# Performance work log

Measured on AMD Instinct MI355X. Metric: run time of the kernel, lower is better.

Reference implementation:

```python
import jax, jax.numpy as jnp
import numpy as np

EPS = 1e-8  # torch.cosine_similarity eps
TEMPERATURE = 1.0


def setup_inputs() -> dict:
    key = jax.random.key(0)
    ks = jax.random.split(key, 12)
    B = 16384
    inp = {
        "user_ids": jax.random.randint(ks[0], (B, 8), 0, 100000),
        "item_ids": jax.random.randint(ks[1], (B, 4), 0, 50000),
        "sample_weight": jax.random.uniform(ks[2], (B,), jnp.float32, 0.01, 1.0),
        "user_table": jax.random.normal(ks[3], (100000, 64), jnp.float32) * 0.05,
        "item_table": jax.random.normal(ks[4], (50000, 64), jnp.float32) * 0.05,
        "uW1": jax.random.normal(ks[5], (512, 256), jnp.float32) * 0.04,
        "ub1": jnp.zeros((256,), jnp.float32),
        "uW2": jax.random.normal(ks[6], (256, 128), jnp.float32) * 0.06,
        "ub2": jnp.zeros((128,), jnp.float32),
        "iW1": jax.random.normal(ks[7], (256, 256), jnp.float32) * 0.06,
        "ib1": jnp.zeros((256,), jnp.float32),
        "iW2": jax.random.normal(ks[8], (256, 128), jnp.float32) * 0.06,
        "ib2": jnp.zeros((128,), jnp.float32),
        "n_neg": 3,
    }
    return inp


def _tower(ids, table, W1, b1, W2, b2):
    # embedding lookup [B, F, D] -> concat -> [B, F*D], then 2-layer relu MLP
    B = ids.shape[0]
    e = table[ids].reshape(B, -1)
    h = jax.nn.relu(e @ W1 + b1)
    return jax.nn.relu(h @ W2 + b2)


def reference(user_ids, item_ids, sample_weight, user_table, item_table,
              uW1, ub1, uW2, ub2, iW1, ib1, iW2, ib2, n_neg):
    u = _tower(user_ids, user_table, uW1, ub1, uW2, ub2)  # [B, 128]
    v = _tower(item_ids, item_table, iW1, ib1, iW2, ib2)  # [B, 128]
    # cosine similarity per row (torch eps clamp on norms)
    un = jnp.maximum(jnp.linalg.norm(u, axis=1), EPS)
    vn = jnp.maximum(jnp.linalg.norm(v, axis=1), EPS)
    y = jnp.sum(u * v, axis=1) / (un * vn)
    # sampling-bias correction
    y = y - jnp.log(sample_weight)
    # vectorized wrap-around in-batch negative gather:
    # scores[i] = [y[i], y[(i+1)%B], ..., y[(i+n_neg)%B]]
    B = y.shape[0]
    idx = (jnp.arange(B)[:, None] + jnp.arange(n_neg + 1)[None, :]) % B
    scores = y[idx] / TEMPERATURE  # [B, 1+n_neg]
    return scores
```

## Files before the change

### kernel.cpp

```cpp
#include <hip/hip_runtime.h>
#include <math.h>

#define CEPS 1e-8f

typedef __attribute__((ext_vector_type(8))) short bf16x8;
typedef __attribute__((ext_vector_type(4))) float f32x4;
typedef __attribute__((ext_vector_type(4))) unsigned int u32x4;

__device__ __forceinline__ unsigned short f2bf(float f) {
    unsigned u = __builtin_bit_cast(unsigned, f);
    u += 0x7fffu + ((u >> 16) & 1u);
    return (unsigned short)(u >> 16);
}

__global__ __launch_bounds__(256)
void pack_all(const float* __restrict__ uW1, const float* __restrict__ uW2,
              const float* __restrict__ iW1, const float* __restrict__ iW2,
              unsigned short* __restrict__ o1, unsigned short* __restrict__ o2,
              unsigned short* __restrict__ o3, unsigned short* __restrict__ o4)
{
    int g = blockIdx.x * 256 + threadIdx.x;
    const float* src; unsigned short* dst; int N; int base;
    if (g < 16384)      { src = uW1; dst = o1; N = 256; base = 0;     }
    else if (g < 20480) { src = uW2; dst = o2; N = 128; base = 16384; }
    else if (g < 28672) { src = iW1; dst = o3; N = 256; base = 20480; }
    else                { src = iW2; dst = o4; N = 128; base = 28672; }
    int i = g - base;
    int kg = i / N, n = i - kg * N;
    unsigned short tmp[8];
    #pragma unroll
    for (int j = 0; j < 8; ++j)
        tmp[j] = f2bf(src[(kg * 8 + j) * N + n]);
    *reinterpret_cast<bf16x8*>(dst + ((size_t)i << 3)) =
        *reinterpret_cast<bf16x8*>(tmp);
}


template<int F>
__device__ __forceinline__ void stage_emb(const int* __restrict__ ids,
                                          const float* __restrict__ table,
                                          unsigned short* e_s, int row0, int tid)
{
    constexpr int FC = F * 8;
    constexpr int IT = (64 * FC) / 1024;
    int idv[IT];
    #pragma unroll
    for (int it = 0; it < IT; ++it) {
        int c = tid + it * 1024;
        int r = c / FC, f = (c % FC) >> 3;
        idv[it] = ids[(row0 + r) * F + f];
    }
    #pragma unroll
    for (int it = 0; it < IT; ++it) {
        int c = tid + it * 1024;
        int r = c / FC, rem = c % FC, ci = rem & 7;
        const float* src = table + (size_t)idv[it] * 64 + ci * 8;
        float4 aa = *reinterpret_cast<const float4*>(src);
        float4 bb = *reinterpret_cast<const float4*>(src + 4);
        u32x4 pk;
        pk.x = f2bf(aa.x) | ((unsigned)f2bf(aa.y) << 16);
        pk.y = f2bf(aa.z) | ((unsigned)f2bf(aa.w) << 16);
        pk.z = f2bf(bb.x) | ((unsigned)f2bf(bb.y) << 16);
        pk.w = f2bf(bb.z) | ((unsigned)f2bf(bb.w) << 16);
        int byte = r * (F * 128) + rem * 16;
        byte ^= (r & 7) << 4;
        *reinterpret_cast<u32x4*>(reinterpret_cast<char*>(e_s) + byte) = pk;
    }
}

template<int KB>
__device__ __forceinline__ bf16x8 loadA(const unsigned short* s, int rowbase,
                                        int ks, int m, int l15, int l4)
{
    int row = rowbase + m * 16 + l15;
    int byte = row * (KB * 2) + ks * 64 + l4 * 16;
    byte ^= (row & 7) << 4;
    return *reinterpret_cast<const bf16x8*>(
               reinterpret_cast<const char*>(s) + byte);
}

template<int K1>
__device__ __forceinline__ void gemm1(
    const unsigned short* e_s, unsigned short* h_s,
    const unsigned short* __restrict__ W1p, const float* __restrict__ b1,
    int l15, int l4, int w, bf16x8 b0)
{
    constexpr int NKS = K1 / 32;
    const int col = w * 16 + l15;
    f32x4 acc[4];
    #pragma unroll
    for (int m = 0; m < 4; ++m) acc[m] = (f32x4){0.f, 0.f, 0.f, 0.f};

    const unsigned short* Wbase = W1p + (((l4 * 256) + col) << 3);
    bf16x8 aB[2][4], bB[2];
    bB[0] = b0;
    #pragma unroll
    for (int m = 0; m < 4; ++m) aB[0][m] = loadA<K1>(e_s, 0, 0, m, l15, l4);

    #pragma unroll
    for (int ks = 0; ks < NKS; ++ks) {
        const int cur = ks & 1, nxt = cur ^ 1;
        if (ks + 1 < NKS) {
            #pragma unroll
            for (int m = 0; m < 4; ++m)
                aB[nxt][m] = loadA<K1>(e_s, 0, ks + 1, m, l15, l4);
            bB[nxt] = *reinterpret_cast<const bf16x8*>(Wbase + (ks + 1) * 8192);
        }
        #pragma unroll
        for (int m = 0; m < 4; ++m)
            acc[m] = __builtin_amdgcn_mfma_f32_16x16x32_bf16(
                         aB[cur][m], bB[cur], acc[m], 0, 0, 0);
    }
    const float bias = b1[col];
    #pragma unroll
    for (int m = 0; m < 4; ++m)
        #pragma unroll
        for (int r = 0; r < 4; ++r) {
            int row = m * 16 + l4 * 4 + r;
            float v = acc[m][r] + bias;
            v = v > 0.f ? v : 0.f;
            int byte = (row * 256 + col) * 2;
            byte ^= (row & 7) << 4;
            *reinterpret_cast<unsigned short*>(
                reinterpret_cast<char*>(h_s) + byte) = f2bf(v);
        }
}

__device__ __forceinline__ void gemm2(
    const unsigned short* h_s, const unsigned short* __restrict__ W2p,
    f32x4 (&acc)[2], int l15, int l4, int w, bf16x8 b0)
{
    const int col = (w & 7) * 16 + l15;
    const int rowbase = (w >> 3) * 32;
    #pragma unroll
    for (int m = 0; m < 2; ++m) acc[m] = (f32x4){0.f, 0.f, 0.f, 0.f};

    const unsigned short* Wbase = W2p + (((l4 * 128) + col) << 3);
    bf16x8 aB[2][2], bB[2];
    bB[0] = b0;
    #pragma unroll
    for (int m = 0; m < 2; ++m) aB[0][m] = loadA<256>(h_s, rowbase, 0, m, l15, l4);

    #pragma unroll
    for (int ks = 0; ks < 8; ++ks) {
        const int cur = ks & 1, nxt = cur ^ 1;
        if (ks + 1 < 8) {
            #pragma unroll
            for (int m = 0; m < 2; ++m)
                aB[nxt][m] = loadA<256>(h_s, rowbase, ks + 1, m, l15, l4);
            bB[nxt] = *reinterpret_cast<const bf16x8*>(Wbase + (ks + 1) * 4096);
        }
        #pragma unroll
        for (int m = 0; m < 2; ++m)
            acc[m] = __builtin_amdgcn_mfma_f32_16x16x32_bf16(
                         aB[cur][m], bB[cur], acc[m], 0, 0, 0);
    }
}

__global__ __launch_bounds__(1024, 4)
void fused_sbc(const int* __restrict__ user_ids,  const int* __restrict__ item_ids,
               const float* __restrict__ user_table, const float* __restrict__ item_table,
               const unsigned short* __restrict__ uW1p, const float* __restrict__ ub1,
               const unsigned short* __restrict__ uW2p, const float* __restrict__ ub2,
               const unsigned short* __restrict__ iW1p, const float* __restrict__ ib1,
               const unsigned short* __restrict__ iW2p, const float* __restrict__ ib2,
               const float* __restrict__ sw, float* __restrict__ out,
               int B, int nn1)
{
    __shared__ unsigned short e_u[64 * 512];
    __shared__ unsigned short e_i[64 * 256];
    __shared__ unsigned short h_s[64 * 256];
    __shared__ float red[8][64][3];

    const int tid  = threadIdx.x;
    const int lane = tid & 63;
    const int w    = tid >> 6;
    const int l15  = lane & 15, l4 = lane >> 4;
    const int row0 = blockIdx.x * 64;

    bf16x8 b0u1 = *reinterpret_cast<const bf16x8*>(
                      uW1p + ((l4 * 256 + w * 16 + l15) << 3));
    stage_emb<8>(user_ids, user_table, e_u, row0, tid);
    stage_emb<4>(item_ids, item_table, e_i, row0, tid);
    __syncthreads();

    gemm1<512>(e_u, h_s, uW1p, ub1, l15, l4, w, b0u1);
    bf16x8 b0u2 = *reinterpret_cast<const bf16x8*>(
                      uW2p + ((l4 * 128 + (w & 7) * 16 + l15) << 3));
    bf16x8 b0i1 = *reinterpret_cast<const bf16x8*>(
                      iW1p + ((l4 * 256 + w * 16 + l15) << 3));
    __syncthreads();

    f32x4 accU[2];
    gemm2(h_s, uW2p, accU, l15, l4, w, b0u2);
    __syncthreads();

    gemm1<256>(e_i, h_s, iW1p, ib1, l15, l4, w, b0i1);
    bf16x8 b0i2 = *reinterpret_cast<const bf16x8*>(
                      iW2p + ((l4 * 128 + (w & 7) * 16 + l15) << 3));
    __syncthreads();

    f32x4 accV[2];
    gemm2(h_s, iW2p, accV, l15, l4, w, b0i2);

    const int col = (w & 7) * 16 + l15;
    const float bu = ub2[col];
    const float bv = ib2[col];
    float pd[8], pu[8], pv[8];
    #pragma unroll
    for (int m = 0; m < 2; ++m)
        #pragma unroll
        for (int r = 0; r < 4; ++r) {
            float uval = accU[m][r] + bu;
            float vval = accV[m][r] + bv;
            uval = uval > 0.f ? uval : 0.f;
            vval = vval > 0.f ? vval : 0.f;
            int i = m * 4 + r;
            pd[i] = uval * vval;
            pu[i] = uval * uval;
            pv[i] = vval * vval;
        }
    #pragma unroll
    for (int off = 1; off < 16; off <<= 1) {
        #pragma unroll
        for (int i = 0; i < 8; ++i) {
            pd[i] += __shfl_xor(pd[i], off);
            pu[i] += __shfl_xor(pu[i], off);
            pv[i] += __shfl_xor(pv[i], off);
        }
    }
    if (l15 == 0) {
        const int rowbase = (w >> 3) * 32;
        #pragma unroll
        for (int m = 0; m < 2; ++m)
            #pragma unroll
            for (int r = 0; r < 4; ++r) {
                int row = rowbase + m * 16 + l4 * 4 + r;
                int i = m * 4 + r;
                red[w & 7][row][0] = pd[i];
                red[w & 7][row][1] = pu[i];
                red[w & 7][row][2] = pv[i];
            }
    }
    __syncthreads();

    if (tid < 64) {
        int row = tid;
        float d = 0.f, su = 0.f, sv = 0.f;
        #pragma unroll
        for (int cg = 0; cg < 8; ++cg) {
            d  += red[cg][row][0];
            su += red[cg][row][1];
            sv += red[cg][row][2];
        }
        float un = fmaxf(sqrtf(su), CEPS);
        float vn = fmaxf(sqrtf(sv), CEPS);
        int grow = row0 + row;
        float yv = d / (un * vn) - logf(sw[grow]);
        for (int j = 0; j < nn1; ++j) {
            int idx = grow - j;
            if (idx < 0) idx += B;
            out[idx * nn1 + j] = yv;
        }
    }
}

extern "C" void kernel_launch(void* const* d_in, const int* in_sizes, int n_in,
                              void* d_out, int out_size, void* d_ws, size_t ws_size,
                              hipStream_t stream)
{
    const int*   user_ids   = (const int*)  d_in[0];
    const int*   item_ids   = (const int*)  d_in[1];
    const float* sw         = (const float*)d_in[2];
    const float* user_table = (const float*)d_in[3];
    const float* item_table = (const float*)d_in[4];
    const float* uW1        = (const float*)d_in[5];
    const float* ub1        = (const float*)d_in[6];
    const float* uW2        = (const float*)d_in[7];
    const float* ub2        = (const float*)d_in[8];
    const float* iW1        = (const float*)d_in[9];
    const float* ib1        = (const float*)d_in[10];
    const float* iW2        = (const float*)d_in[11];
    const float* ib2        = (const float*)d_in[12];

    const int B   = in_sizes[2];
    const int nn1 = out_size / B;

    unsigned short* wp   = (unsigned short*)d_ws;
    unsigned short* uW1p = wp;
    unsigned short* uW2p = wp + 131072;
    unsigned short* iW1p = wp + 163840;
    unsigned short* iW2p = wp + 229376;
    float* out = (float*)d_out;

    pack_all<<<128, 256, 0, stream>>>(uW1, uW2, iW1, iW2,
                                      uW1p, uW2p, iW1p, iW2p);
    fused_sbc<<<B / 64, 1024, 0, stream>>>(user_ids, item_ids,
                                           user_table, item_table,
                                           uW1p, ub1, uW2p, ub2,
                                           iW1p, ib1, iW2p, ib2,
                                           sw, out, B, nn1);
}
```

Before: 33.57 us.

## Run user and item towers concurrently on separate wave halves

Splits the 16 waves into two roles: waves 0-7 run the user tower and waves 8-15 run the item tower at the same time, each on its own hidden buffer. Each wave now computes a wider tile (32 columns in layer 1, all 64 rows in layer 2), and the item tower output is passed to the user waves through LDS for the dot product. This removes two block-wide barriers and the serial user-then-item schedule, and gives each wave more MFMAs per A-fragment load. In exchange it uses more registers, drops the 4-blocks occupancy hint, and leaves the two towers with unequal work (K of 512 versus 256), so the item waves may sit idle.

Result: faster. 32.40 us (-3.5%).

```diff
diff --git a/kernel.cpp b/kernel.cpp
--- a/kernel.cpp
+++ b/kernel.cpp
@@ -69,10 +69,10 @@
 }
 
 template<int KB>
-__device__ __forceinline__ bf16x8 loadA(const unsigned short* s, int rowbase,
-                                        int ks, int m, int l15, int l4)
-{
-    int row = rowbase + m * 16 + l15;
+__device__ __forceinline__ bf16x8 loadA(const unsigned short* s, int ks, int m,
+                                        int l15, int l4)
+{
+    int row = m * 16 + l15;
     int byte = row * (KB * 2) + ks * 64 + l4 * 16;
     byte ^= (row & 7) << 4;
     return *reinterpret_cast<const bf16x8*>(
@@ -83,19 +83,22 @@
 __device__ __forceinline__ void gemm1(
     const unsigned short* e_s, unsigned short* h_s,
     const unsigned short* __restrict__ W1p, const float* __restrict__ b1,
-    int l15, int l4, int w, bf16x8 b0)
+    int l15, int l4, int wl, const bf16x8* b0)
 {
     constexpr int NKS = K1 / 32;
-    const int col = w * 16 + l15;
-    f32x4 acc[4];
-    #pragma unroll
-    for (int m = 0; m < 4; ++m) acc[m] = (f32x4){0.f, 0.f, 0.f, 0.f};
-
-    const unsigned short* Wbase = W1p + (((l4 * 256) + col) << 3);
-    bf16x8 aB[2][4], bB[2];
-    bB[0] = b0;
-    #pragma unroll
-    for (int m = 0; m < 4; ++m) aB[0][m] = loadA<K1>(e_s, 0, 0, m, l15, l4);
+    const int colbase = wl * 32;
+    f32x4 acc[4][2];
+    #pragma unroll
+    for (int m = 0; m < 4; ++m)
+        #pragma unroll
+        for (int n = 0; n < 2; ++n) acc[m][n] = (f32x4){0.f, 0.f, 0.f, 0.f};
+
+    const unsigned short* Wbase = W1p + (((l4 * 256) + colbase + l15) << 3);
+    bf16x8 aB[2][4], bB[2][2];
+    bB[0][0] = b0[0];
+    bB[0][1] = b0[1];
+    #pragma unroll
+    for (int m = 0; m < 4; ++m) aB[0][m] = loadA<K1>(e_s, 0, m, l15, l4);
 
     #pragma unroll
     for (int ks = 0; ks < NKS; ++ks) {
@@ -103,61 +106,69 @@
         if (ks + 1 < NKS) {
             #pragma unroll
             for (int m = 0; m < 4; ++m)
-                aB[nxt][m] = loadA<K1>(e_s, 0, ks + 1, m, l15, l4);
-            bB[nxt] = *reinterpret_cast<const bf16x8*>(Wbase + (ks + 1) * 8192);
+                aB[nxt][m] = loadA<K1>(e_s, ks + 1, m, l15, l4);
+            #pragma unroll
+            for (int n = 0; n < 2; ++n)
+                bB[nxt][n] = *reinterpret_cast<const bf16x8*>(
+                                 Wbase + (ks + 1) * 8192 + (n << 7));
+        }
+        #pragma unroll
+        for (int n = 0; n < 2; ++n)
+            #pragma unroll
+            for (int m = 0; m < 4; ++m)
+                acc[m][n] = __builtin_amdgcn_mfma_f32_16x16x32_bf16(
+                                aB[cur][m], bB[cur][n], acc[m][n], 0, 0, 0);
+    }
+    #pragma unroll
+    for (int n = 0; n < 2; ++n) {
+        int col = colbase + n * 16 + l15;
+        float bias = b1[col];
+        #pragma unroll
+        for (int m = 0; m < 4; ++m)
+            #pragma unroll
+            for (int r = 0; r < 4; ++r) {
+                int row = m * 16 + l4 * 4 + r;
+                float v = acc[m][n][r] + bias;
+                v = v > 0.f ? v : 0.f;
+                int byte = (row * 256 + col) * 2;
+                byte ^= (row & 7) << 4;
+                *reinterpret_cast<unsigned short*>(
+                    reinterpret_cast<char*>(h_s) + byte) = f2bf(v);
+            }
+    }
+}
+
+__device__ __forceinline__ void gemm2(
+    const unsigned short* h_s, const unsigned short* __restrict__ W2p,
+    f32x4 (&acc)[4], int l15, int l4, int wl, bf16x8 b0)
+{
+    const int col = wl * 16 + l15;
+    #pragma unroll
+    for (int m = 0; m < 4; ++m) acc[m] = (f32x4){0.f, 0.f, 0.f, 0.f};
+
+    const unsigned short* Wbase = W2p + (((l4 * 128) + col) << 3);
+    bf16x8 aB[2][4], bB[2];
+    bB[0] = b0;
+    #pragma unroll
+    for (int m = 0; m < 4; ++m) aB[0][m] = loadA<256>(h_s, 0, m, l15, l4);
+
+    #pragma unroll
+    for (int ks = 0; ks < 8; ++ks) {
+        const int cur = ks & 1, nxt = cur ^ 1;
+        if (ks + 1 < 8) {
+            #pragma unroll
+            for (int m = 0; m < 4; ++m)
+                aB[nxt][m] = loadA<256>(h_s, ks + 1, m, l15, l4);
+            bB[nxt] = *reinterpret_cast<const bf16x8*>(Wbase + (ks + 1) * 4096);
         }
         #pragma unroll
         for (int m = 0; m < 4; ++m)
             acc[m] = __builtin_amdgcn_mfma_f32_16x16x32_bf16(
                          aB[cur][m], bB[cur], acc[m], 0, 0, 0);
     }
-    const float bias = b1[col];
-    #pragma unroll
-    for (int m = 0; m < 4; ++m)
-        #pragma unroll
-        for (int r = 0; r < 4; ++r) {
-            int row = m * 16 + l4 * 4 + r;
-            float v = acc[m][r] + bias;
-            v = v > 0.f ? v : 0.f;
-            int byte = (row * 256 + col) * 2;
-            byte ^= (row & 7) << 4;
-            *reinterpret_cast<unsigned short*>(
-                reinterpret_cast<char*>(h_s) + byte) = f2bf(v);
-        }
-}
-
-__device__ __forceinline__ void gemm2(
-    const unsigned short* h_s, const unsigned short* __restrict__ W2p,
-    f32x4 (&acc)[2], int l15, int l4, int w, bf16x8 b0)
-{
-    const int col = (w & 7) * 16 + l15;
-    const int rowbase = (w >> 3) * 32;
-    #pragma unroll
-    for (int m = 0; m < 2; ++m) acc[m] = (f32x4){0.f, 0.f, 0.f, 0.f};
-
-    const unsigned short* Wbase = W2p + (((l4 * 128) + col) << 3);
-    bf16x8 aB[2][2], bB[2];
-    bB[0] = b0;
-    #pragma unroll
-    for (int m = 0; m < 2; ++m) aB[0][m] = loadA<256>(h_s, rowbase, 0, m, l15, l4);
-
-    #pragma unroll
-    for (int ks = 0; ks < 8; ++ks) {
-        const int cur = ks & 1, nxt = cur ^ 1;
-        if (ks + 1 < 8) {
-            #pragma unroll
-            for (int m = 0; m < 2; ++m)
-                aB[nxt][m] = loadA<256>(h_s, rowbase, ks + 1, m, l15, l4);
-            bB[nxt] = *reinterpret_cast<const bf16x8*>(Wbase + (ks + 1) * 4096);
-        }
-        #pragma unroll
-        for (int m = 0; m < 2; ++m)
-            acc[m] = __builtin_amdgcn_mfma_f32_16x16x32_bf16(
-                         aB[cur][m], bB[cur], acc[m], 0, 0, 0);
-    }
-}
-
-__global__ __launch_bounds__(1024, 4)
+}
+
+__global__ __launch_bounds__(1024)
 void fused_sbc(const int* __restrict__ user_ids,  const int* __restrict__ item_ids,
                const float* __restrict__ user_table, const float* __restrict__ item_table,
                const unsigned short* __restrict__ uW1p, const float* __restrict__ ub1,
@@ -167,80 +178,108 @@
                const float* __restrict__ sw, float* __restrict__ out,
                int B, int nn1)
 {
-    __shared__ unsigned short e_u[64 * 512];
-    __shared__ unsigned short e_i[64 * 256];
-    __shared__ unsigned short h_s[64 * 256];
-    __shared__ float red[8][64][3];
+    __shared__ __align__(16) unsigned short smem[81920];
+    unsigned short* e_u = smem;
+    unsigned short* e_i = smem + 32768;
+    unsigned short* h_u = smem + 49152;
+    unsigned short* h_i = smem + 65536;
+    float* V_lds = reinterpret_cast<float*>(smem);
+    float* red   = reinterpret_cast<float*>(smem + 32768);
 
     const int tid  = threadIdx.x;
     const int lane = tid & 63;
     const int w    = tid >> 6;
     const int l15  = lane & 15, l4 = lane >> 4;
+    const int role = w >> 3;
+    const int wl   = w & 7;
     const int row0 = blockIdx.x * 64;
 
-    bf16x8 b0u1 = *reinterpret_cast<const bf16x8*>(
-                      uW1p + ((l4 * 256 + w * 16 + l15) << 3));
+    const unsigned short* W1sel = role ? iW1p : uW1p;
+    const unsigned short* W2sel = role ? iW2p : uW2p;
+
+    bf16x8 b0g1[2];
+    {
+        const unsigned short* base = W1sel + ((l4 * 256 + wl * 32 + l15) << 3);
+        b0g1[0] = *reinterpret_cast<const bf16x8*>(base);
+        b0g1[1] = *reinterpret_cast<const bf16x8*>(base + 128);
+    }
     stage_emb<8>(user_ids, user_table, e_u, row0, tid);
     stage_emb<4>(item_ids, item_table, e_i, row0, tid);
     __syncthreads();
 
-    gemm1<512>(e_u, h_s, uW1p, ub1, l15, l4, w, b0u1);
-    bf16x8 b0u2 = *reinterpret_cast<const bf16x8*>(
-                      uW2p + ((l4 * 128 + (w & 7) * 16 + l15) << 3));
-    bf16x8 b0i1 = *reinterpret_cast<const bf16x8*>(
-                      iW1p + ((l4 * 256 + w * 16 + l15) << 3));
+    if (role == 0) gemm1<512>(e_u, h_u, uW1p, ub1, l15, l4, wl, b0g1);
+    else           gemm1<256>(e_i, h_i, iW1p, ib1, l15, l4, wl, b0g1);
+    bf16x8 b0g2 = *reinterpret_cast<const bf16x8*>(
+                      W2sel + ((l4 * 128 + wl * 16 + l15) << 3));
     __syncthreads();
 
-    f32x4 accU[2];
-    gemm2(h_s, uW2p, accU, l15, l4, w, b0u2);
+    f32x4 acc2[4];
+    if (role == 0) gemm2(h_u, uW2p, acc2, l15, l4, wl, b0g2);
+    else           gemm2(h_i, iW2p, acc2, l15, l4, wl, b0g2);
+
+    const int col = wl * 16 + l15;
+
+    if (role == 1) {
+        const float bv = ib2[col];
+        float pv[16];
+        #pragma unroll
+        for (int m = 0; m < 4; ++m)
+            #pragma unroll
+            for (int r = 0; r < 4; ++r) {
+                float vv = acc2[m][r] + bv;
+                vv = vv > 0.f ? vv : 0.f;
+                int row = m * 16 + l4 * 4 + r;
+                V_lds[row * 132 + col] = vv;
+                pv[m * 4 + r] = vv * vv;
+            }
+        #pragma unroll
+        for (int off = 1; off < 16; off <<= 1)
+            #pragma unroll
+            for (int i = 0; i < 16; ++i)
+                pv[i] += __shfl_xor(pv[i], off);
+        if (l15 == 0) {
+            #pragma unroll
+            for (int m = 0; m < 4; ++m)
+                #pragma unroll
+                for (int r = 0; r < 4; ++r) {
+                    int row = m * 16 + l4 * 4 + r;
+                    red[(wl * 64 + row) * 3 + 2] = pv[m * 4 + r];
+                }
+        }
+    }
     __syncthreads();
 
-    gemm1<256>(e_i, h_s, iW1p, ib1, l15, l4, w, b0i1);
-    bf16x8 b0i2 = *reinterpret_cast<const bf16x8*>(
-                      iW2p + ((l4 * 128 + (w & 7) * 16 + l15) << 3));
-    __syncthreads();
-
-    f32x4 accV[2];
-    gemm2(h_s, iW2p, accV, l15, l4, w, b0i2);
-
-    const int col = (w & 7) * 16 + l15;
-    const float bu = ub2[col];
-    const float bv = ib2[col];
-    float pd[8], pu[8], pv[8];
-    #pragma unroll
-    for (int m = 0; m < 2; ++m)
-        #pragma unroll
-        for (int r = 0; r < 4; ++r) {
-            float uval = accU[m][r] + bu;
-            float vval = accV[m][r] + bv;
-            uval = uval > 0.f ? uval : 0.f;
-            vval = vval > 0.f ? vval : 0.f;
-            int i = m * 4 + r;
-            pd[i] = uval * vval;
-            pu[i] = uval * uval;
-            pv[i] = vval * vval;
-        }
-    #pragma unroll
-    for (int off = 1; off < 16; off <<= 1) {
-        #pragma unroll
-        for (int i = 0; i < 8; ++i) {
-            pd[i] += __shfl_xor(pd[i], off);
-            pu[i] += __shfl_xor(pu[i], off);
-            pv[i] += __shfl_xor(pv[i], off);
-        }
-    }
-    if (l15 == 0) {
-        const int rowbase = (w >> 3) * 32;
-        #pragma unroll
-        for (int m = 0; m < 2; ++m)
+    if (role == 0) {
+        const float bu = ub2[col];
+        float pd[16], pu[16];
+        #pragma unroll
+        for (int m = 0; m < 4; ++m)
             #pragma unroll
             for (int r = 0; r < 4; ++r) {
-                int row = rowbase + m * 16 + l4 * 4 + r;
-                int i = m * 4 + r;
-                red[w & 7][row][0] = pd[i];
-                red[w & 7][row][1] = pu[i];
-                red[w & 7][row][2] = pv[i];
+                float uu = acc2[m][r] + bu;
+                uu = uu > 0.f ? uu : 0.f;
+                int row = m * 16 + l4 * 4 + r;
+                float vv = V_lds[row * 132 + col];
+                pd[m * 4 + r] = uu * vv;
+                pu[m * 4 + r] = uu * uu;
             }
+        #pragma unroll
+        for (int off = 1; off < 16; off <<= 1)
+            #pragma unroll
+            for (int i = 0; i < 16; ++i) {
+                pd[i] += __shfl_xor(pd[i], off);
+                pu[i] += __shfl_xor(pu[i], off);
+            }
+        if (l15 == 0) {
+            #pragma unroll
+            for (int m = 0; m < 4; ++m)
+                #pragma unroll
+                for (int r = 0; r < 4; ++r) {
+                    int row = m * 16 + l4 * 4 + r;
+                    red[(wl * 64 + row) * 3 + 0] = pd[m * 4 + r];
+                    red[(wl * 64 + row) * 3 + 1] = pu[m * 4 + r];
+                }
+        }
     }
     __syncthreads();
 
@@ -249,9 +288,9 @@
         float d = 0.f, su = 0.f, sv = 0.f;
         #pragma unroll
         for (int cg = 0; cg < 8; ++cg) {
-            d  += red[cg][row][0];
-            su += red[cg][row][1];
-            sv += red[cg][row][2];
+            d  += red[(cg * 64 + row) * 3 + 0];
+            su += red[(cg * 64 + row) * 3 + 1];
+            sv += red[(cg * 64 + row) * 3 + 2];
         }
         float un = fmaxf(sqrtf(su), CEPS);
         float vn = fmaxf(sqrtf(sv), CEPS);
```

## Shrink fused tower tile to 16 rows with swapped MFMA operands and smaller LDS

Applied to the files above, without the earlier changes.

Cuts the per-block tile from 64 rows/1024 threads to 16 rows/512 threads and swaps the MFMA operands so weights fill the M dimension and batch rows fill N. This shrinks LDS use, raises blocks per CU and the total grid size, and lets bias loads be vectorised. The item gather is held in registers, and LDS buffers are reused between the user and item towers. It also adds a three-deep weight prefetch and s_setprio around the MFMAs. In exchange, each weight fragment is reused across only 16 rows, so global/L2 weight traffic per output row roughly quadruples.

Measured after the change: 36.97 us. 1.1x slower.

```diff
diff --git a/kernel.cpp b/kernel.cpp
--- a/kernel.cpp
+++ b/kernel.cpp
@@ -6,6 +6,7 @@
 typedef __attribute__((ext_vector_type(8))) short bf16x8;
 typedef __attribute__((ext_vector_type(4))) float f32x4;
 typedef __attribute__((ext_vector_type(4))) unsigned int u32x4;
+typedef __attribute__((ext_vector_type(2))) unsigned int u32x2;
 
 __device__ __forceinline__ unsigned short f2bf(float f) {
     unsigned u = __builtin_bit_cast(unsigned, f);
@@ -36,45 +37,12 @@
 }
 
 
-template<int F>
-__device__ __forceinline__ void stage_emb(const int* __restrict__ ids,
-                                          const float* __restrict__ table,
-                                          unsigned short* e_s, int row0, int tid)
-{
-    constexpr int FC = F * 8;
-    constexpr int IT = (64 * FC) / 1024;
-    int idv[IT];
-    #pragma unroll
-    for (int it = 0; it < IT; ++it) {
-        int c = tid + it * 1024;
-        int r = c / FC, f = (c % FC) >> 3;
-        idv[it] = ids[(row0 + r) * F + f];
-    }
-    #pragma unroll
-    for (int it = 0; it < IT; ++it) {
-        int c = tid + it * 1024;
-        int r = c / FC, rem = c % FC, ci = rem & 7;
-        const float* src = table + (size_t)idv[it] * 64 + ci * 8;
-        float4 aa = *reinterpret_cast<const float4*>(src);
-        float4 bb = *reinterpret_cast<const float4*>(src + 4);
-        u32x4 pk;
-        pk.x = f2bf(aa.x) | ((unsigned)f2bf(aa.y) << 16);
-        pk.y = f2bf(aa.z) | ((unsigned)f2bf(aa.w) << 16);
-        pk.z = f2bf(bb.x) | ((unsigned)f2bf(bb.y) << 16);
-        pk.w = f2bf(bb.z) | ((unsigned)f2bf(bb.w) << 16);
-        int byte = r * (F * 128) + rem * 16;
-        byte ^= (r & 7) << 4;
-        *reinterpret_cast<u32x4*>(reinterpret_cast<char*>(e_s) + byte) = pk;
-    }
-}
-
 template<int KB>
-__device__ __forceinline__ bf16x8 loadA(const unsigned short* s, int rowbase,
-                                        int ks, int m, int l15, int l4)
-{
-    int row = rowbase + m * 16 + l15;
-    int byte = row * (KB * 2) + ks * 64 + l4 * 16;
-    byte ^= (row & 7) << 4;
+__device__ __forceinline__ bf16x8 loadA(const unsigned short* s, int ks,
+                                        int l15, int l4)
+{
+    int byte = l15 * (KB * 2) + ks * 64 + l4 * 16;
+    byte ^= (l15 & 7) << 4;
     return *reinterpret_cast<const bf16x8*>(
                reinterpret_cast<const char*>(s) + byte);
 }
@@ -83,81 +51,83 @@
 __device__ __forceinline__ void gemm1(
     const unsigned short* e_s, unsigned short* h_s,
     const unsigned short* __restrict__ W1p, const float* __restrict__ b1,
-    int l15, int l4, int w, bf16x8 b0)
+    int l15, int l4, int wl)
 {
     constexpr int NKS = K1 / 32;
-    const int col = w * 16 + l15;
-    f32x4 acc[4];
-    #pragma unroll
-    for (int m = 0; m < 4; ++m) acc[m] = (f32x4){0.f, 0.f, 0.f, 0.f};
-
-    const unsigned short* Wbase = W1p + (((l4 * 256) + col) << 3);
-    bf16x8 aB[2][4], bB[2];
-    bB[0] = b0;
-    #pragma unroll
-    for (int m = 0; m < 4; ++m) aB[0][m] = loadA<K1>(e_s, 0, 0, m, l15, l4);
+    f32x4 acc[2];
+    acc[0] = (f32x4){0.f, 0.f, 0.f, 0.f};
+    acc[1] = (f32x4){0.f, 0.f, 0.f, 0.f};
+
+    const unsigned short* Wbase = W1p + ((l4 * 256 + wl * 32 + l15) << 3);
+    bf16x8 wf[3][2], ef[2];
+    #pragma unroll
+    for (int mi = 0; mi < 2; ++mi) {
+        wf[0][mi] = *reinterpret_cast<const bf16x8*>(Wbase + (mi << 7));
+        wf[1][mi] = *reinterpret_cast<const bf16x8*>(Wbase + 8192 + (mi << 7));
+    }
+    ef[0] = loadA<K1>(e_s, 0, l15, l4);
 
     #pragma unroll
     for (int ks = 0; ks < NKS; ++ks) {
-        const int cur = ks & 1, nxt = cur ^ 1;
-        if (ks + 1 < NKS) {
+        if (ks + 2 < NKS) {
             #pragma unroll
-            for (int m = 0; m < 4; ++m)
-                aB[nxt][m] = loadA<K1>(e_s, 0, ks + 1, m, l15, l4);
-            bB[nxt] = *reinterpret_cast<const bf16x8*>(Wbase + (ks + 1) * 8192);
-        }
-        #pragma unroll
-        for (int m = 0; m < 4; ++m)
-            acc[m] = __builtin_amdgcn_mfma_f32_16x16x32_bf16(
-                         aB[cur][m], bB[cur], acc[m], 0, 0, 0);
-    }
-    const float bias = b1[col];
-    #pragma unroll
-    for (int m = 0; m < 4; ++m)
-        #pragma unroll
-        for (int r = 0; r < 4; ++r) {
-            int row = m * 16 + l4 * 4 + r;
-            float v = acc[m][r] + bias;
-            v = v > 0.f ? v : 0.f;
-            int byte = (row * 256 + col) * 2;
-            byte ^= (row & 7) << 4;
-            *reinterpret_cast<unsigned short*>(
-                reinterpret_cast<char*>(h_s) + byte) = f2bf(v);
-        }
-}
-
-__device__ __forceinline__ void gemm2(
+            for (int mi = 0; mi < 2; ++mi)
+                wf[(ks + 2) % 3][mi] = *reinterpret_cast<const bf16x8*>(
+                    Wbase + (ks + 2) * 8192 + (mi << 7));
+        }
+        if (ks + 1 < NKS)
+            ef[(ks + 1) & 1] = loadA<K1>(e_s, ks + 1, l15, l4);
+        __builtin_amdgcn_s_setprio(1);
+        #pragma unroll
+        for (int mi = 0; mi < 2; ++mi)
+            acc[mi] = __builtin_amdgcn_mfma_f32_16x16x32_bf16(
+                          wf[ks % 3][mi], ef[ks & 1], acc[mi], 0, 0, 0);
+        __builtin_amdgcn_s_setprio(0);
+    }
+    #pragma unroll
+    for (int mi = 0; mi < 2; ++mi) {
+        const int colb = wl * 32 + mi * 16 + l4 * 4;
+        const float4 bb = *reinterpret_cast<const float4*>(&b1[colb]);
+        float v0 = acc[mi][0] + bb.x; v0 = v0 > 0.f ? v0 : 0.f;
+        float v1 = acc[mi][1] + bb.y; v1 = v1 > 0.f ? v1 : 0.f;
+        float v2 = acc[mi][2] + bb.z; v2 = v2 > 0.f ? v2 : 0.f;
+        float v3 = acc[mi][3] + bb.w; v3 = v3 > 0.f ? v3 : 0.f;
+        u32x2 d;
+        d.x = f2bf(v0) | ((unsigned)f2bf(v1) << 16);
+        d.y = f2bf(v2) | ((unsigned)f2bf(v3) << 16);
+        int byte = (l15 * 256 + colb) * 2;
+        byte ^= (l15 & 7) << 4;
+        *reinterpret_cast<u32x2*>(reinterpret_cast<char*>(h_s) + byte) = d;
+    }
+}
+
+__device__ __forceinline__ f32x4 gemm2(
     const unsigned short* h_s, const unsigned short* __restrict__ W2p,
-    f32x4 (&acc)[2], int l15, int l4, int w, bf16x8 b0)
-{
-    const int col = (w & 7) * 16 + l15;
-    const int rowbase = (w >> 3) * 32;
-    #pragma unroll
-    for (int m = 0; m < 2; ++m) acc[m] = (f32x4){0.f, 0.f, 0.f, 0.f};
-
-    const unsigned short* Wbase = W2p + (((l4 * 128) + col) << 3);
-    bf16x8 aB[2][2], bB[2];
-    bB[0] = b0;
-    #pragma unroll
-    for (int m = 0; m < 2; ++m) aB[0][m] = loadA<256>(h_s, rowbase, 0, m, l15, l4);
+    int l15, int l4, int wl)
+{
+    f32x4 acc = (f32x4){0.f, 0.f, 0.f, 0.f};
+    const unsigned short* Wbase = W2p + ((l4 * 128 + wl * 16 + l15) << 3);
+    bf16x8 wf[3], hf[2];
+    wf[0] = *reinterpret_cast<const bf16x8*>(Wbase);
+    wf[1] = *reinterpret_cast<const bf16x8*>(Wbase + 4096);
+    hf[0] = loadA<256>(h_s, 0, l15, l4);
 
     #pragma unroll
     for (int ks = 0; ks < 8; ++ks) {
-        const int cur = ks & 1, nxt = cur ^ 1;
-        if (ks + 1 < 8) {
-            #pragma unroll
-            for (int m = 0; m < 2; ++m)
-                aB[nxt][m] = loadA<256>(h_s, rowbase, ks + 1, m, l15, l4);
-            bB[nxt] = *reinterpret_cast<const bf16x8*>(Wbase + (ks + 1) * 4096);
-        }
-        #pragma unroll
-        for (int m = 0; m < 2; ++m)
-            acc[m] = __builtin_amdgcn_mfma_f32_16x16x32_bf16(
-                         aB[cur][m], bB[cur], acc[m], 0, 0, 0);
-    }
-}
-
-__global__ __launch_bounds__(1024, 4)
+        if (ks + 2 < 8)
+            wf[(ks + 2) % 3] = *reinterpret_cast<const bf16x8*>(
+                                   Wbase + (ks + 2) * 4096);
+        if (ks + 1 < 8)
+            hf[(ks + 1) & 1] = loadA<256>(h_s, ks + 1, l15, l4);
+        __builtin_amdgcn_s_setprio(1);
+        acc = __builtin_amdgcn_mfma_f32_16x16x32_bf16(
+                  wf[ks % 3], hf[ks & 1], acc, 0, 0, 0);
+        __builtin_amdgcn_s_setprio(0);
+    }
+    return acc;
+}
+
+__global__ __launch_bounds__(512, 6)
 void fused_sbc(const int* __restrict__ user_ids,  const int* __restrict__ item_ids,
                const float* __restrict__ user_table, const float* __restrict__ item_table,
                const unsigned short* __restrict__ uW1p, const float* __restrict__ ub1,
@@ -167,91 +137,113 @@
                const float* __restrict__ sw, float* __restrict__ out,
                int B, int nn1)
 {
-    __shared__ unsigned short e_u[64 * 512];
-    __shared__ unsigned short e_i[64 * 256];
-    __shared__ unsigned short h_s[64 * 256];
-    __shared__ float red[8][64][3];
+    __shared__ __align__(16) unsigned short smem[13056];
+    unsigned short* e_u  = smem;
+    unsigned short* hbuf = smem + 8192;
+    float* red = reinterpret_cast<float*>(smem + 12288);
 
     const int tid  = threadIdx.x;
     const int lane = tid & 63;
-    const int w    = tid >> 6;
+    const int wl   = tid >> 6;
     const int l15  = lane & 15, l4 = lane >> 4;
-    const int row0 = blockIdx.x * 64;
-
-    bf16x8 b0u1 = *reinterpret_cast<const bf16x8*>(
-                      uW1p + ((l4 * 256 + w * 16 + l15) << 3));
-    stage_emb<8>(user_ids, user_table, e_u, row0, tid);
-    stage_emb<4>(item_ids, item_table, e_i, row0, tid);
-    __syncthreads();
-
-    gemm1<512>(e_u, h_s, uW1p, ub1, l15, l4, w, b0u1);
-    bf16x8 b0u2 = *reinterpret_cast<const bf16x8*>(
-                      uW2p + ((l4 * 128 + (w & 7) * 16 + l15) << 3));
-    bf16x8 b0i1 = *reinterpret_cast<const bf16x8*>(
-                      iW1p + ((l4 * 256 + w * 16 + l15) << 3));
-    __syncthreads();
-
-    f32x4 accU[2];
-    gemm2(h_s, uW2p, accU, l15, l4, w, b0u2);
-    __syncthreads();
-
-    gemm1<256>(e_i, h_s, iW1p, ib1, l15, l4, w, b0i1);
-    bf16x8 b0i2 = *reinterpret_cast<const bf16x8*>(
-                      iW2p + ((l4 * 128 + (w & 7) * 16 + l15) << 3));
-    __syncthreads();
-
-    f32x4 accV[2];
-    gemm2(h_s, iW2p, accV, l15, l4, w, b0i2);
-
-    const int col = (w & 7) * 16 + l15;
-    const float bu = ub2[col];
-    const float bv = ib2[col];
-    float pd[8], pu[8], pv[8];
-    #pragma unroll
-    for (int m = 0; m < 2; ++m)
-        #pragma unroll
-        for (int r = 0; r < 4; ++r) {
-            float uval = accU[m][r] + bu;
-            float vval = accV[m][r] + bv;
-            uval = uval > 0.f ? uval : 0.f;
-            vval = vval > 0.f ? vval : 0.f;
-            int i = m * 4 + r;
-            pd[i] = uval * vval;
-            pu[i] = uval * uval;
-            pv[i] = vval * vval;
-        }
-    #pragma unroll
-    for (int off = 1; off < 16; off <<= 1) {
-        #pragma unroll
-        for (int i = 0; i < 8; ++i) {
-            pd[i] += __shfl_xor(pd[i], off);
-            pu[i] += __shfl_xor(pu[i], off);
-            pv[i] += __shfl_xor(pv[i], off);
-        }
-    }
-    if (l15 == 0) {
-        const int rowbase = (w >> 3) * 32;
-        #pragma unroll
-        for (int m = 0; m < 2; ++m)
-            #pragma unroll
-            for (int r = 0; r < 4; ++r) {
-                int row = rowbase + m * 16 + l4 * 4 + r;
-                int i = m * 4 + r;
-                red[w & 7][row][0] = pd[i];
-                red[w & 7][row][1] = pu[i];
-                red[w & 7][row][2] = pv[i];
-            }
-    }
-    __syncthreads();
-
-    if (tid < 64) {
+    const int row0 = blockIdx.x * 16;
+
+    const int r_i = tid >> 5, rem_i = tid & 31;
+    u32x4 ipk;
+    {
+        int f_i = rem_i >> 3, ci = rem_i & 7;
+        int id = item_ids[(row0 + r_i) * 4 + f_i];
+        const float* src = item_table + (size_t)id * 64 + ci * 8;
+        float4 aa = *reinterpret_cast<const float4*>(src);
+        float4 bb = *reinterpret_cast<const float4*>(src + 4);
+        ipk.x = f2bf(aa.x) | ((unsigned)f2bf(aa.y) << 16);
+        ipk.y = f2bf(aa.z) | ((unsigned)f2bf(aa.w) << 16);
+        ipk.z = f2bf(bb.x) | ((unsigned)f2bf(bb.y) << 16);
+        ipk.w = f2bf(bb.z) | ((unsigned)f2bf(bb.w) << 16);
+    }
+
+    {
+        int idv[2];
+        #pragma unroll
+        for (int it = 0; it < 2; ++it) {
+            int c = tid + it * 512;
+            int r = c >> 6, f = (c & 63) >> 3;
+            idv[it] = user_ids[(row0 + r) * 8 + f];
+        }
+        #pragma unroll
+        for (int it = 0; it < 2; ++it) {
+            int c = tid + it * 512;
+            int r = c >> 6, rem = c & 63, ci = rem & 7;
+            const float* src = user_table + (size_t)idv[it] * 64 + ci * 8;
+            float4 aa = *reinterpret_cast<const float4*>(src);
+            float4 bb = *reinterpret_cast<const float4*>(src + 4);
+            u32x4 pk;
+            pk.x = f2bf(aa.x) | ((unsigned)f2bf(aa.y) << 16);
+            pk.y = f2bf(aa.z) | ((unsigned)f2bf(aa.w) << 16);
+            pk.z = f2bf(bb.x) | ((unsigned)f2bf(bb.y) << 16);
+            pk.w = f2bf(bb.z) | ((unsigned)f2bf(bb.w) << 16);
+            int byte = r * 1024 + rem * 16;
+            byte ^= (r & 7) << 4;
+            *reinterpret_cast<u32x4*>(reinterpret_cast<char*>(e_u) + byte) = pk;
+        }
+    }
+    __syncthreads();
+
+    gemm1<512>(e_u, hbuf, uW1p, ub1, l15, l4, wl);
+    __syncthreads();
+    f32x4 au = gemm2(hbuf, uW2p, l15, l4, wl);
+    float u0, u1, u2, u3;
+    {
+        const float4 bu = *reinterpret_cast<const float4*>(
+                              &ub2[wl * 16 + l4 * 4]);
+        u0 = au[0] + bu.x; u0 = u0 > 0.f ? u0 : 0.f;
+        u1 = au[1] + bu.y; u1 = u1 > 0.f ? u1 : 0.f;
+        u2 = au[2] + bu.z; u2 = u2 > 0.f ? u2 : 0.f;
+        u3 = au[3] + bu.w; u3 = u3 > 0.f ? u3 : 0.f;
+    }
+    __syncthreads();
+
+    {
+        int byte = r_i * 512 + rem_i * 16;
+        byte ^= (r_i & 7) << 4;
+        *reinterpret_cast<u32x4*>(reinterpret_cast<char*>(hbuf) + byte) = ipk;
+    }
+    __syncthreads();
+
+    gemm1<256>(hbuf, e_u, iW1p, ib1, l15, l4, wl);
+    __syncthreads();
+    f32x4 av = gemm2(e_u, iW2p, l15, l4, wl);
+    float v0, v1, v2, v3;
+    {
+        const float4 bv = *reinterpret_cast<const float4*>(
+                              &ib2[wl * 16 + l4 * 4]);
+        v0 = av[0] + bv.x; v0 = v0 > 0.f ? v0 : 0.f;
+        v1 = av[1] + bv.y; v1 = v1 > 0.f ? v1 : 0.f;
+        v2 = av[2] + bv.z; v2 = v2 > 0.f ? v2 : 0.f;
+        v3 = av[3] + bv.w; v3 = v3 > 0.f ? v3 : 0.f;
+    }
+
+    float pd = u0 * v0 + u1 * v1 + u2 * v2 + u3 * v3;
+    float pu = u0 * u0 + u1 * u1 + u2 * u2 + u3 * u3;
+    float pv = v0 * v0 + v1 * v1 + v2 * v2 + v3 * v3;
+    pd += __shfl_xor(pd, 16); pd += __shfl_xor(pd, 32);
+    pu += __shfl_xor(pu, 16); pu += __shfl_xor(pu, 32);
+    pv += __shfl_xor(pv, 16); pv += __shfl_xor(pv, 32);
+    if (l4 == 0) {
+        red[(wl * 16 + l15) * 3 + 0] = pd;
+        red[(wl * 16 + l15) * 3 + 1] = pu;
+        red[(wl * 16 + l15) * 3 + 2] = pv;
+    }
+    __syncthreads();
+
+    if (tid < 16) {
         int row = tid;
         float d = 0.f, su = 0.f, sv = 0.f;
         #pragma unroll
         for (int cg = 0; cg < 8; ++cg) {
-            d  += red[cg][row][0];
-            su += red[cg][row][1];
-            sv += red[cg][row][2];
+            d  += red[(cg * 16 + row) * 3 + 0];
+            su += red[(cg * 16 + row) * 3 + 1];
+            sv += red[(cg * 16 + row) * 3 + 2];
         }
         float un = fmaxf(sqrtf(su), CEPS);
         float vn = fmaxf(sqrtf(sv), CEPS);
@@ -295,9 +287,9 @@
 
     pack_all<<<128, 256, 0, stream>>>(uW1, uW2, iW1, iW2,
                                       uW1p, uW2p, iW1p, iW2p);
-    fused_sbc<<<B / 64, 1024, 0, stream>>>(user_ids, item_ids,
-                                           user_table, item_table,
-                                           uW1p, ub1, uW2p, ub2,
-                                           iW1p, ib1, iW2p, ib2,
-                                           sw, out, B, nn1);
-}
+    fused_sbc<<<B / 16, 512, 0, stream>>>(user_ids, item_ids,
+                                          user_table, item_table,
+                                          uW1p, ub1, uW2p, ub2,
+                                          iW1p, ib1, iW2p, ib2,
+                                          sw, out, B, nn1);
+}
```
